# Optimization experiments

Measured on AMD Instinct MI355X. Metric: run time of the kernel, lower is better.

Reference implementation:

```python
import jax, jax.numpy as jnp
import numpy as np

BITS = 8
EPS = 1e-5
NUM_HEADS = 16


def quantize_weight(w, eps=EPS):
    # per-tensor abs-mean scale, ternary weights in {-1, 0, 1}
    scale = jnp.maximum(jnp.mean(jnp.abs(w)), eps)
    qw = jnp.clip(jnp.round(w / scale), -1.0, 1.0)
    return qw, scale


def bitlinear158_inference(x, qw, scale, bias=None, bits=BITS, eps=EPS):
    # per-token abs-max activation quantization to [-Q, Q-1]
    q = float(2 ** (bits - 1))
    gamma = jnp.maximum(jnp.max(jnp.abs(x), axis=-1, keepdims=True), eps)
    qx = jnp.clip(jnp.round(x * (q / gamma)), -q, q - 1.0)
    out = jnp.einsum('...i,oi->...o', qx, qw)
    out = out * (scale * gamma / q)
    if bias is not None:
        out = out + bias
    return out


def setup_inputs() -> dict:
    rng = jax.random.key(0)
    ks = jax.random.split(rng, 7)
    B, L, E = 4, 2048, 1024
    return {
        'query': jax.random.normal(ks[0], (B, L, E), jnp.float32),
        'key': jax.random.normal(ks[1], (B, L, E), jnp.float32),
        'value': jax.random.normal(ks[2], (B, L, E), jnp.float32),
        'in_proj_weight': jax.random.normal(ks[3], (3 * E, E), jnp.float32) * 0.02,
        'in_proj_bias': jax.random.normal(ks[4], (3 * E,), jnp.float32) * 0.02,
        'out_proj_weight': jax.random.normal(ks[5], (E, E), jnp.float32) * 0.02,
        'out_proj_bias': jax.random.normal(ks[6], (E,), jnp.float32) * 0.02,
    }


def reference(query, key, value, in_proj_weight, in_proj_bias, out_proj_weight, out_proj_bias):
    B, Lq, E = query.shape
    Lk = key.shape[1]
    H = NUM_HEADS
    D = E // H

    # quantize weights as done at __init__ time
    qw, kw, vw = jnp.split(in_proj_weight, 3, axis=0)  # each [E, E]
    qb, kb, vb = jnp.split(in_proj_bias, 3, axis=0)
    q_qw, q_s = quantize_weight(qw)
    k_qw, k_s = quantize_weight(kw)
    v_qw, v_s = quantize_weight(vw)
    o_qw, o_s = quantize_weight(out_proj_weight)

    # quantized projections [B, L, E]
    q = bitlinear158_inference(query, q_qw, q_s, qb)
    k = bitlinear158_inference(key, k_qw, k_s, kb)
    v = bitlinear158_inference(value, v_qw, v_s, vb)

    # [B, H, L, D]
    q = q.reshape(B, Lq, H, D).transpose(0, 2, 1, 3)
    k = k.reshape(B, Lk, H, D).transpose(0, 2, 1, 3)
    v = v.reshape(B, Lk, H, D).transpose(0, 2, 1, 3)

    scores = jnp.einsum('bhqd,bhkd->bhqk', q, k) / jnp.sqrt(jnp.asarray(D, q.dtype))
    attn = jax.nn.softmax(scores, axis=-1)
    ctx = jnp.einsum('bhqk,bhkd->bhqd', attn, v)  # [B, H, Lq, D]
    ctx = ctx.transpose(0, 2, 1, 3).reshape(B, Lq, E)

    out = bitlinear158_inference(ctx, o_qw, o_s, out_proj_bias)
    return out
```

## Files before the change

### kernel.cpp

```cpp
#include <hip/hip_runtime.h>
#include <cstdint>
#include <cstddef>

#define BB 4
#define LL 2048
#define EE 1024
#define HH 16
#define DD 64
#define TT (BB*LL)
#define EPSF 1e-5f

typedef _Float16 half8 __attribute__((ext_vector_type(8)));
typedef _Float16 half4v __attribute__((ext_vector_type(4)));
typedef float floatx4 __attribute__((ext_vector_type(4)));
typedef float floatx16 __attribute__((ext_vector_type(16)));
typedef int intx4 __attribute__((ext_vector_type(4)));
typedef unsigned int uintx4 __attribute__((ext_vector_type(4)));
typedef unsigned int uint2v __attribute__((ext_vector_type(2)));

__device__ __forceinline__ void gl_lds16(const void* g, void* l) {
    __builtin_amdgcn_global_load_lds(
        (const __attribute__((address_space(1))) void*)g,
        (__attribute__((address_space(3))) void*)l, 16, 0, 0);
}

__device__ __forceinline__ uint32_t pk2(float a, float b) {
    union { _Float16 h[2]; uint32_t u; } x;
    x.h[0] = (_Float16)a; x.h[1] = (_Float16)b;
    return x.u;
}

__global__ void k_absum(const float* __restrict__ in_proj,
                        const float* __restrict__ out_proj,
                        double* __restrict__ sums) {
    const int which = blockIdx.y;
    const float* src = (which < 3) ? (in_proj + (size_t)which * EE * EE) : out_proj;
    double loc = 0.0;
    const int n = EE * EE;
    for (int i = blockIdx.x * blockDim.x + threadIdx.x; i < n; i += gridDim.x * blockDim.x)
        loc += (double)fabsf(src[i]);
    #pragma unroll
    for (int off = 32; off > 0; off >>= 1) loc += __shfl_down(loc, off, 64);
    __shared__ double red[4];
    const int lane = threadIdx.x & 63, wv = threadIdx.x >> 6;
    if (lane == 0) red[wv] = loc;
    __syncthreads();
    if (threadIdx.x == 0) {
        double tot = red[0] + red[1] + red[2] + red[3];
        atomicAdd(&sums[which], tot);
    }
}

__global__ void k_quantw(const float* __restrict__ in_proj,
                         const float* __restrict__ out_proj,
                         const double* __restrict__ sums,
                         float* __restrict__ scaleF,
                         int8_t* __restrict__ qw) {
    const int idx = blockIdx.x * blockDim.x + threadIdx.x;
    if (idx < 4) scaleF[idx] = fmaxf((float)(sums[idx] * (1.0 / (EE * EE))), EPSF);
    const int which = idx >> 20;
    const float s = fmaxf((float)(sums[which] * (1.0 / (EE * EE))), EPSF);
    const float w = (which < 3) ? in_proj[idx] : out_proj[idx - 3 * EE * EE];
    float q = rintf(w / s);
    q = fminf(fmaxf(q, -1.f), 1.f);
    qw[idx] = (int8_t)q;
}

__device__ __forceinline__ void gammaq_body(const float* __restrict__ x,
                                            float* __restrict__ g,
                                            int8_t* __restrict__ qx) {
    const int wv = threadIdx.x >> 6, lane = threadIdx.x & 63;
    const int tok = blockIdx.x * 4 + wv;
    const float* xp = x + (size_t)tok * EE;
    float4 v[4];
    #pragma unroll
    for (int i = 0; i < 4; i++) v[i] = *(const float4*)(xp + (lane + 64 * i) * 4);
    float m = 0.f;
    #pragma unroll
    for (int i = 0; i < 4; i++)
        m = fmaxf(m, fmaxf(fmaxf(fabsf(v[i].x), fabsf(v[i].y)),
                           fmaxf(fabsf(v[i].z), fabsf(v[i].w))));
    #pragma unroll
    for (int off = 1; off < 64; off <<= 1) m = fmaxf(m, __shfl_xor(m, off, 64));
    const float gg = fmaxf(m, EPSF);
    const float rg = 128.f / gg;
    int8_t* qp = qx + (size_t)tok * EE;
    #pragma unroll
    for (int i = 0; i < 4; i++) {
        char4 c;
        c.x = (int8_t)(int)fminf(fmaxf(rintf(v[i].x * rg), -128.f), 127.f);
        c.y = (int8_t)(int)fminf(fmaxf(rintf(v[i].y * rg), -128.f), 127.f);
        c.z = (int8_t)(int)fminf(fmaxf(rintf(v[i].z * rg), -128.f), 127.f);
        c.w = (int8_t)(int)fminf(fmaxf(rintf(v[i].w * rg), -128.f), 127.f);
        *(char4*)(qp + (lane + 64 * i) * 4) = c;
    }
    if (lane == 0) g[tok] = gg;
}

__global__ __launch_bounds__(256) void k_gammaq3(const float* __restrict__ q,
                                                 const float* __restrict__ k,
                                                 const float* __restrict__ v,
                                                 float* __restrict__ g,
                                                 int8_t* __restrict__ qx) {
    const int y = blockIdx.y;
    const float* src = (y == 0) ? q : (y == 1) ? k : v;
    gammaq_body(src, g + (size_t)y * TT, qx + (size_t)y * TT * EE);
}

__global__ __launch_bounds__(256) void k_gammaq(const float* __restrict__ x,
                                                float* __restrict__ g,
                                                int8_t* __restrict__ qx) {
    gammaq_body(x, g, qx);
}

__global__ __launch_bounds__(256) void k_bitmm(
    const int8_t* __restrict__ qx_all, const float* __restrict__ gam_all,
    const int8_t* __restrict__ qw_all, const float* __restrict__ scaleF,
    const float* __restrict__ in_proj_b, const float* __restrict__ out_proj_b,
    float* __restrict__ outF, _Float16* __restrict__ outH_all,
    int wbase, float qpre) {
    __shared__ __align__(16) int8_t smem[36864];
    int8_t (*As)[128] = (int8_t(*)[128])smem;
    int8_t (*Bs)[128] = (int8_t(*)[128])(smem + 16384);
    _Float16 (*Vt)[136] = (_Float16(*)[136])smem;
    const int widx = wbase + blockIdx.z;
    const int8_t* qx = qx_all + (size_t)widx * TT * EE;
    const int8_t* qw = qw_all + (size_t)widx * EE * EE;
    const float* gam = gam_all + (size_t)widx * TT;
    const float* bias = (widx < 3) ? (in_proj_b + widx * EE) : out_proj_b;
    _Float16* outH = outH_all + (size_t)widx * TT * EE;
    const float pre = (widx == 0) ? qpre : 1.0f;
    const int tid = threadIdx.x;
    const int wv = tid >> 6, lane = tid & 63;
    const int quad = lane >> 4, l16 = lane & 15;
    const int wm = wv & 1, wn = wv >> 1;
    const int t0 = blockIdx.x * 128, o0 = blockIdx.y * 128;
    const int srow = lane >> 3, schunk = lane & 7;

    intx4 acc[4][4];
    #pragma unroll
    for (int i = 0; i < 4; i++)
        #pragma unroll
        for (int j = 0; j < 4; j++) acc[i][j] = (intx4){0, 0, 0, 0};

    for (int k0 = 0; k0 < EE; k0 += 128) {
        __syncthreads();
        #pragma unroll
        for (int p = 0; p < 4; p++) {
            const int g = wv * 4 + p;
            const int c = schunk ^ srow ^ (g & 7);
            const int row = g * 8 + srow;
            gl_lds16(qx + (size_t)(t0 + row) * EE + k0 + c * 16, &As[g * 8][0]);
            gl_lds16(qw + (size_t)(o0 + row) * EE + k0 + c * 16, &Bs[g * 8][0]);
        }
        __syncthreads();
        #pragma unroll
        for (int kk = 0; kk < 2; kk++) {
            intx4 af[4], bf[4];
            #pragma unroll
            for (int s4 = 0; s4 < 4; s4++) {
                const int mR = (l16 & 7) ^ ((s4 * 2 + (l16 >> 3)) & 7);
                const int ph = ((kk * 4 + quad) ^ mR) * 16;
                af[s4] = *(const intx4*)&As[wm * 64 + s4 * 16 + l16][ph];
                bf[s4] = *(const intx4*)&Bs[wn * 64 + s4 * 16 + l16][ph];
            }
            #pragma unroll
            for (int sm = 0; sm < 4; sm++)
                #pragma unroll
                for (int sn = 0; sn < 4; sn++)
                    acc[sm][sn] = __builtin_amdgcn_mfma_i32_16x16x64_i8(
                        af[sm], bf[sn], acc[sm][sn], 0, 0, 0);
        }
    }

    const float s = scaleF[widx];
    if (widx == 2) {
        __syncthreads();
        #pragma unroll
        for (int sm = 0; sm < 4; sm++) {
            const int tl = wm * 64 + sm * 16 + quad * 4;
            float mr[4];
            #pragma unroll
            for (int r = 0; r < 4; r++) mr[r] = s * gam[t0 + tl + r] * 0.0078125f;
            #pragma unroll
            for (int sn = 0; sn < 4; sn++) {
                const int ol = wn * 64 + sn * 16 + l16;
                const float b = bias[o0 + ol];
                half4v hv;
                #pragma unroll
                for (int r = 0; r < 4; r++)
                    hv[r] = (_Float16)((float)acc[sm][sn][r] * mr[r] + b);
                *(half4v*)&Vt[ol][tl] = hv;
            }
        }
        __syncthreads();
        const int ol2 = tid >> 1, tc0 = (tid & 1) * 64;
        const int og = o0 + ol2, hh = og >> 6, dd = og & 63;
        const int bb = t0 >> 11, l0 = t0 & (LL - 1);
        _Float16* dst = outH + ((size_t)(bb * HH + hh) * DD + dd) * LL + l0 + tc0;
        #pragma unroll
        for (int i = 0; i < 8; i++)
            *(half8*)(dst + i * 8) = *(const half8*)&Vt[ol2][tc0 + i * 8];
        return;
    }
    #pragma unroll
    for (int sm = 0; sm < 4; sm++) {
        #pragma unroll
        for (int r = 0; r < 4; r++) {
            const int t = t0 + wm * 64 + sm * 16 + quad * 4 + r;
            const float mr = s * gam[t] * 0.0078125f;
            const int b_ = t >> 11, l_ = t & (LL - 1);
            #pragma unroll
            for (int sn = 0; sn < 4; sn++) {
                const int o = o0 + wn * 64 + sn * 16 + l16;
                const float val = (float)acc[sm][sn][r] * mr + bias[o];
                if (widx == 3) {
                    outF[(size_t)t * EE + o] = val;
                } else {
                    const int h_ = o >> 6, d_ = o & 63;
                    outH[((size_t)(b_ * HH + h_) * LL + l_) * DD + d_] = (_Float16)(val * pre);
                }
            }
        }
    }
}

__global__ __launch_bounds__(256, 4) void k_attn5(const _Float16* __restrict__ Q,
                                                  const _Float16* __restrict__ K,
                                                  const _Float16* __restrict__ Vt,
                                                  float* __restrict__ ctx) {
    __shared__ __align__(16) _Float16 Ksh[2][64][64];
    __shared__ __align__(16) _Float16 Vtsh[2][64][64];
    const int tid = threadIdx.x;
    const int wv = tid >> 6, lane = tid & 63;
    const int l32 = lane & 31, h2 = lane >> 5;
    const int bh = blockIdx.y, b_ = bh >> 4, h_ = bh & 15;
    const int q0 = blockIdx.x * 128 + wv * 32;
    const int srow = lane >> 3, schunk = lane & 7;

    const _Float16* Qb = Q + (size_t)bh * LL * DD;
    const _Float16* Kb = K + (size_t)bh * LL * DD;
    const _Float16* Vtb = Vt + (size_t)bh * DD * LL;

    half8 qf[4];
    #pragma unroll
    for (int ds = 0; ds < 4; ds++)
        qf[ds] = *(const half8*)(Qb + (size_t)(q0 + l32) * DD + ds * 16 + h2 * 8);

    floatx16 acc[2];
    #pragma unroll
    for (int r = 0; r < 16; r++) { acc[0][r] = 0.f; acc[1][r] = 0.f; }
    float lsum = 0.f;

    {
        #pragma unroll
        for (int u = 0; u < 2; u++) {
            const int g = wv * 2 + u;
            const int c = schunk ^ srow ^ (g & 7);
            const int row = g * 8 + srow;
            gl_lds16(Kb + (size_t)row * DD + c * 8, &Ksh[0][g * 8][0]);
            gl_lds16(Vtb + (size_t)row * LL + c * 8, &Vtsh[0][g * 8][0]);
        }
    }
    __syncthreads();

    for (int kt = 0; kt < LL; kt += 64) {
        const int cur = (kt >> 6) & 1;

        if (kt + 64 < LL) {
            const int nkt = kt + 64;
            #pragma unroll
            for (int u = 0; u < 2; u++) {
                const int g = wv * 2 + u;
                const int c = schunk ^ srow ^ (g & 7);
                const int row = g * 8 + srow;
                gl_lds16(Kb + (size_t)(nkt + row) * DD + c * 8, &Ksh[cur ^ 1][g * 8][0]);
                gl_lds16(Vtb + (size_t)row * LL + nkt + c * 8, &Vtsh[cur ^ 1][g * 8][0]);
            }
        }

        half8 pa[4];
        #pragma unroll
        for (int ks = 0; ks < 2; ks++) {
            const int rowK = ks * 32 + l32;
            const int mK = (l32 & 7) ^ ((ks * 4 + (l32 >> 3)) & 7);
            floatx16 sc;
            #pragma unroll
            for (int r = 0; r < 16; r++) sc[r] = 0.f;
            __builtin_amdgcn_s_setprio(1);
            #pragma unroll
            for (int ds = 0; ds < 4; ds++) {
                const half8 kf = *(const half8*)&Ksh[cur][rowK][((2 * ds + h2) ^ mK) * 8];
                sc = __builtin_amdgcn_mfma_f32_32x32x16_f16(kf, qf[ds], sc, 0, 0, 0);
            }
            __builtin_amdgcn_s_setprio(0);
            float p[16];
            #pragma unroll
            for (int r = 0; r < 16; r++) p[r] = __builtin_amdgcn_exp2f(sc[r]);
            #pragma unroll
            for (int r = 0; r < 16; r++) lsum += p[r];
            uint32_t u_[4][2];
            #pragma unroll
            for (int c4 = 0; c4 < 4; c4++) {
                u_[c4][0] = pk2(p[4 * c4 + 0], p[4 * c4 + 1]);
                u_[c4][1] = pk2(p[4 * c4 + 2], p[4 * c4 + 3]);
            }
            #pragma unroll
            for (int mm = 0; mm < 2; mm++) {
                uint2v s0 = __builtin_amdgcn_permlane32_swap(
                    u_[2 * mm][0], u_[2 * mm + 1][0], false, false);
                uint2v s1 = __builtin_amdgcn_permlane32_swap(
                    u_[2 * mm][1], u_[2 * mm + 1][1], false, false);
                uintx4 w;
                w[0] = s0[0]; w[1] = s1[0]; w[2] = s0[1]; w[3] = s1[1];
                union { uintx4 u; half8 h; } cv; cv.u = w;
                pa[ks * 2 + mm] = cv.h;
            }
        }

        __builtin_amdgcn_s_setprio(1);
        #pragma unroll
        for (int kb = 0; kb < 4; kb++) {
            #pragma unroll
            for (int sd = 0; sd < 2; sd++) {
                const int rowV = sd * 32 + l32;
                const int mV = (l32 & 7) ^ ((sd * 4 + (l32 >> 3)) & 7);
                const half8 vf = *(const half8*)&Vtsh[cur][rowV][((2 * kb + h2) ^ mV) * 8];
                acc[sd] = __builtin_amdgcn_mfma_f32_32x32x16_f16(pa[kb], vf, acc[sd], 0, 0, 0);
            }
        }
        __builtin_amdgcn_s_setprio(0);

        __syncthreads();
    }

    lsum += __shfl_xor(lsum, 32, 64);
    const float invl = 1.f / lsum;
    #pragma unroll
    for (int r = 0; r < 16; r++) {
        const int qrow = (r & 3) + 8 * (r >> 2) + 4 * h2;
        const float iv = __shfl(invl, qrow, 64);
        float* cp = ctx + ((size_t)b_ * LL + q0 + qrow) * EE + h_ * DD + l32;
        cp[0]  = acc[0][r] * iv;
        cp[32] = acc[1][r] * iv;
    }
}

extern "C" void kernel_launch(void* const* d_in, const int* in_sizes, int n_in,
                              void* d_out, int out_size, void* d_ws, size_t ws_size,
                              hipStream_t stream) {
    const float* query      = (const float*)d_in[0];
    const float* key        = (const float*)d_in[1];
    const float* value      = (const float*)d_in[2];
    const float* in_proj_w  = (const float*)d_in[3];
    const float* in_proj_b  = (const float*)d_in[4];
    const float* out_proj_w = (const float*)d_in[5];
    const float* out_proj_b = (const float*)d_in[6];
    float* out = (float*)d_out;

    char* ws = (char*)d_ws;
    double*   sums   = (double*)ws;
    float*    scaleF = (float*)(ws + 32);
    float*    gbuf   = (float*)(ws + 256);
    int8_t*   qw8    = (int8_t*)(ws + (size_t)1  * 1024 * 1024);
    int8_t*   qx8    = (int8_t*)(ws + (size_t)8  * 1024 * 1024);
    _Float16* Qh     = (_Float16*)(ws + (size_t)40 * 1024 * 1024);
    _Float16* Kh     = Qh + (size_t)TT * EE;
    _Float16* Vth    = Kh + (size_t)TT * EE;
    float*    ctx    = out;

    const float QPRE = 0.18033688011112042f;

    hipMemsetAsync(sums, 0, 32, stream);
    k_absum<<<dim3(64, 4), 256, 0, stream>>>(in_proj_w, out_proj_w, sums);
    k_quantw<<<(4 * EE * EE) / 256, 256, 0, stream>>>(in_proj_w, out_proj_w, sums, scaleF, qw8);
    k_gammaq3<<<dim3(TT / 4, 3), 256, 0, stream>>>(query, key, value, gbuf, qx8);

    k_bitmm<<<dim3(TT / 128, EE / 128, 3), 256, 0, stream>>>(
        qx8, gbuf, qw8, scaleF, in_proj_b, out_proj_b, nullptr, Qh, 0, QPRE);

    k_attn5<<<dim3(LL / 128, BB * HH), 256, 0, stream>>>(Qh, Kh, Vth, ctx);

    k_gammaq<<<TT / 4, 256, 0, stream>>>(ctx, gbuf + 3 * TT, qx8 + 3 * (size_t)TT * EE);
    k_bitmm<<<dim3(TT / 128, EE / 128, 1), 256, 0, stream>>>(
        qx8, gbuf, qw8, scaleF, in_proj_b, out_proj_b, out, Qh, 3, QPRE);
}
```

Measured before the change: 343.1 us.

## Remap attention blocks to XCDs, compute softmax row sums via MFMA

The attention launch becomes a 1D grid and block IDs are remapped so that all query blocks of a (batch, head) pair land on the same XCD, which should improve L2 reuse of K/V tiles. The per-row softmax denominator now comes from an extra MFMA of the probability fragments against a vector of ones, replacing the scalar accumulation, the cross-lane shuffle and the broadcast. The fp16 packing switches to the hardware round-toward-zero pack instruction, and the first score MFMA uses a zero vector in place of a zeroed accumulator. The costs are one extra MFMA per k-block, a row sum built from fp16-rounded probabilities, and slightly different rounding of those probabilities.

Result: no change. 340.5 us (-0.8%).

```diff
diff --git a/kernel.cpp b/kernel.cpp
--- a/kernel.cpp
+++ b/kernel.cpp
@@ -28,6 +28,10 @@
     union { _Float16 h[2]; uint32_t u; } x;
     x.h[0] = (_Float16)a; x.h[1] = (_Float16)b;
     return x.u;
+}
+
+__device__ __forceinline__ uint32_t pkrtz(float a, float b) {
+    return __builtin_bit_cast(uint32_t, __builtin_amdgcn_cvt_pkrtz(a, b));
 }
 
 __global__ void k_absum(const float* __restrict__ in_proj,
@@ -234,8 +238,12 @@
     const int tid = threadIdx.x;
     const int wv = tid >> 6, lane = tid & 63;
     const int l32 = lane & 31, h2 = lane >> 5;
-    const int bh = blockIdx.y, b_ = bh >> 4, h_ = bh & 15;
-    const int q0 = blockIdx.x * 128 + wv * 32;
+    const int bid = blockIdx.x;
+    const int xcd = bid & 7, j = bid >> 3;
+    const int bh = (xcd << 3) | (j >> 4);
+    const int qblk = j & 15;
+    const int b_ = bh >> 4, h_ = bh & 15;
+    const int q0 = qblk * 128 + wv * 32;
     const int srow = lane >> 3, schunk = lane & 7;
 
     const _Float16* Qb = Q + (size_t)bh * LL * DD;
@@ -247,10 +255,12 @@
     for (int ds = 0; ds < 4; ds++)
         qf[ds] = *(const half8*)(Qb + (size_t)(q0 + l32) * DD + ds * 16 + h2 * 8);
 
-    floatx16 acc[2];
-    #pragma unroll
-    for (int r = 0; r < 16; r++) { acc[0][r] = 0.f; acc[1][r] = 0.f; }
-    float lsum = 0.f;
+    floatx16 acc[2], accl, zv;
+    #pragma unroll
+    for (int r = 0; r < 16; r++) { acc[0][r] = 0.f; acc[1][r] = 0.f; accl[r] = 0.f; zv[r] = 0.f; }
+    half8 ones;
+    #pragma unroll
+    for (int r = 0; r < 8; r++) ones[r] = (_Float16)1.0f;
 
     {
         #pragma unroll
@@ -284,12 +294,14 @@
         for (int ks = 0; ks < 2; ks++) {
             const int rowK = ks * 32 + l32;
             const int mK = (l32 & 7) ^ ((ks * 4 + (l32 >> 3)) & 7);
+            __builtin_amdgcn_s_setprio(1);
             floatx16 sc;
-            #pragma unroll
-            for (int r = 0; r < 16; r++) sc[r] = 0.f;
-            __builtin_amdgcn_s_setprio(1);
-            #pragma unroll
-            for (int ds = 0; ds < 4; ds++) {
+            {
+                const half8 kf = *(const half8*)&Ksh[cur][rowK][((2 * 0 + h2) ^ mK) * 8];
+                sc = __builtin_amdgcn_mfma_f32_32x32x16_f16(kf, qf[0], zv, 0, 0, 0);
+            }
+            #pragma unroll
+            for (int ds = 1; ds < 4; ds++) {
                 const half8 kf = *(const half8*)&Ksh[cur][rowK][((2 * ds + h2) ^ mK) * 8];
                 sc = __builtin_amdgcn_mfma_f32_32x32x16_f16(kf, qf[ds], sc, 0, 0, 0);
             }
@@ -297,13 +309,11 @@
             float p[16];
             #pragma unroll
             for (int r = 0; r < 16; r++) p[r] = __builtin_amdgcn_exp2f(sc[r]);
-            #pragma unroll
-            for (int r = 0; r < 16; r++) lsum += p[r];
             uint32_t u_[4][2];
             #pragma unroll
             for (int c4 = 0; c4 < 4; c4++) {
-                u_[c4][0] = pk2(p[4 * c4 + 0], p[4 * c4 + 1]);
-                u_[c4][1] = pk2(p[4 * c4 + 2], p[4 * c4 + 3]);
+                u_[c4][0] = pkrtz(p[4 * c4 + 0], p[4 * c4 + 1]);
+                u_[c4][1] = pkrtz(p[4 * c4 + 2], p[4 * c4 + 3]);
             }
             #pragma unroll
             for (int mm = 0; mm < 2; mm++) {
@@ -328,18 +338,17 @@
                 const half8 vf = *(const half8*)&Vtsh[cur][rowV][((2 * kb + h2) ^ mV) * 8];
                 acc[sd] = __builtin_amdgcn_mfma_f32_32x32x16_f16(pa[kb], vf, acc[sd], 0, 0, 0);
             }
+            accl = __builtin_amdgcn_mfma_f32_32x32x16_f16(pa[kb], ones, accl, 0, 0, 0);
         }
         __builtin_amdgcn_s_setprio(0);
 
         __syncthreads();
     }
 
-    lsum += __shfl_xor(lsum, 32, 64);
-    const float invl = 1.f / lsum;
     #pragma unroll
     for (int r = 0; r < 16; r++) {
         const int qrow = (r & 3) + 8 * (r >> 2) + 4 * h2;
-        const float iv = __shfl(invl, qrow, 64);
+        const float iv = 1.f / accl[r];
         float* cp = ctx + ((size_t)b_ * LL + q0 + qrow) * EE + h_ * DD + l32;
         cp[0]  = acc[0][r] * iv;
         cp[32] = acc[1][r] * iv;
@@ -379,7 +388,7 @@
     k_bitmm<<<dim3(TT / 128, EE / 128, 3), 256, 0, stream>>>(
         qx8, gbuf, qw8, scaleF, in_proj_b, out_proj_b, nullptr, Qh, 0, QPRE);
 
-    k_attn5<<<dim3(LL / 128, BB * HH), 256, 0, stream>>>(Qh, Kh, Vth, ctx);
+    k_attn5<<<dim3((LL / 128) * BB * HH), 256, 0, stream>>>(Qh, Kh, Vth, ctx);
 
     k_gammaq<<<TT / 4, 256, 0, stream>>>(ctx, gbuf + 3 * TT, qx8 + 3 * (size_t)TT * EE);
     k_bitmm<<<dim3(TT / 128, EE / 128, 1), 256, 0, stream>>>(
```
